# Kernel tuning notes

Measured on AMD Instinct MI355X. Metric: run time of the kernel, lower is better.

Reference implementation:

```python
import jax, jax.numpy as jnp
import numpy as np

N = 100000      # num nodes
E = 1000000     # num edges
R = 50          # num relations
B = 2           # num bases (hard-coded in source)
IN, HID, OUT = 128, 64, 64


def setup_inputs() -> dict:
    key = jax.random.key(0)
    ks = jax.random.split(key, 12)
    def xavier(k, shape):
        fan_in, fan_out = shape[-2], shape[-1]
        lim = (6.0 / (fan_in + fan_out)) ** 0.5
        return jax.random.uniform(k, shape, jnp.float32, -lim, lim)
    return {
        "node_emb": xavier(ks[0], (N, IN)),
        "basis1": xavier(ks[1], (B, IN, HID)),
        "comp1": xavier(ks[2], (R, B)),
        "loop_w1": xavier(ks[3], (IN, HID)),
        "bias1": jnp.zeros((HID,), jnp.float32),
        "basis2": xavier(ks[4], (B, HID, OUT)),
        "comp2": xavier(ks[5], (R, B)),
        "loop_w2": xavier(ks[6], (HID, OUT)),
        "bias2": jnp.zeros((OUT,), jnp.float32),
        "src": jax.random.randint(ks[7], (E,), 0, N, jnp.int32),
        "dst": jax.random.randint(ks[8], (E,), 0, N, jnp.int32),
        "etypes": jax.random.randint(ks[9], (E,), 0, R, jnp.int32),
    }


def _rel_graph_conv(h, basis, comp, loop_w, bias, src, dst, etypes, act):
    # Basis-decomposed R-GCN layer (DGL RelGraphConv, regularizer='basis'):
    #   W_r = sum_b comp[r,b] * basis[b];  m_e = W_{etype_e} h_{src_e}
    # Low-rank form: project with each basis first (2 dense GEMMs), then mix
    # per-edge with the relation coefficients, then scatter-add by dst.
    hb = jnp.einsum('nd,bdo->nbo', h, basis)          # [N, B, out]
    c = comp[etypes]                                   # [E, B]
    msg = jnp.einsum('eb,ebo->eo', c, hb[src])         # gather [E,B,out] -> [E,out]
    agg = jax.ops.segment_sum(msg, dst, num_segments=h.shape[0])  # scatter-add
    return act(agg + h @ loop_w + bias)                # self-loop + bias + activation


def reference(node_emb, basis1, comp1, loop_w1, bias1,
              basis2, comp2, loop_w2, bias2, src, dst, etypes):
    h = _rel_graph_conv(node_emb, basis1, comp1, loop_w1, bias1,
                        src, dst, etypes, jnp.tanh)
    out = _rel_graph_conv(h, basis2, comp2, loop_w2, bias2,
                          src, dst, etypes, jax.nn.relu)
    return out
```

## Files before the change

kernel.cpp:

```cpp
#include <hip/hip_runtime.h>
#include <math.h>


typedef short          short8 __attribute__((ext_vector_type(8)));
typedef float          f32x4  __attribute__((ext_vector_type(4)));
typedef unsigned short u16;

#define NCHUNK 256

static __device__ __forceinline__ u16 bf16_rne(float x) {
    unsigned u = __float_as_uint(x);
    return (u16)((u + 0x7fffu + ((u >> 16) & 1u)) >> 16);
}
static __device__ __forceinline__ float bf16_f32(u16 h) {
    return __uint_as_float(((unsigned)h) << 16);
}

__device__ __forceinline__ void wconv_body(
    int tid,
    const float* __restrict__ loopw1, const float* __restrict__ basis1,
    const float* __restrict__ loopw2, const float* __restrict__ basis2,
    u16* __restrict__ wt1h, u16* __restrict__ wt1l,
    u16* __restrict__ wt2h, u16* __restrict__ wt2l)
{
    if (tid < 192 * 128) {
        const int j = tid >> 7, k = tid & 127;
        const float w = (j < 64)
            ? loopw1[k * 64 + j]
            : basis1[(size_t)((j - 64) >> 6) * (128 * 64) + k * 64 + ((j - 64) & 63)];
        const u16 h = bf16_rne(w);
        wt1h[tid] = h;
        wt1l[tid] = bf16_rne(w - bf16_f32(h));
    }
    if (tid < 192 * 64) {
        const int j = tid >> 6, k = tid & 63;
        const float w = (j < 64)
            ? loopw2[k * 64 + j]
            : basis2[(size_t)((j - 64) >> 6) * (64 * 64) + k * 64 + ((j - 64) & 63)];
        const u16 h = bf16_rne(w);
        wt2h[tid] = h;
        wt2l[tid] = bf16_rne(w - bf16_f32(h));
    }
}

__global__ __launch_bounds__(256) void prep_count(
    const int* __restrict__ dst, int* __restrict__ cnt, int nE, int nB,
    const float* __restrict__ loopw1, const float* __restrict__ basis1,
    const float* __restrict__ loopw2, const float* __restrict__ basis2,
    u16* __restrict__ wt1h, u16* __restrict__ wt1l,
    u16* __restrict__ wt2h, u16* __restrict__ wt2l)
{
    const int t = threadIdx.x;
    if (blockIdx.x >= NCHUNK) {
        wconv_body((blockIdx.x - NCHUNK) * 256 + t,
                   loopw1, basis1, loopw2, basis2, wt1h, wt1l, wt2h, wt2l);
        return;
    }
    __shared__ int lh[1024];
    for (int b = t; b < 1024; b += 256) lh[b] = 0;
    __syncthreads();
    const int chunk = (nE + NCHUNK - 1) / NCHUNK;
    const int e0 = blockIdx.x * chunk;
    const int e1 = min(nE, e0 + chunk);
    for (int e = e0 + t; e < e1; e += 256)
        atomicAdd(&lh[dst[e] >> 7], 1);
    __syncthreads();
    for (int b = t; b < nB; b += 256)
        cnt[blockIdx.x * nB + b] = lh[b];
}

template<int K>
__global__ __launch_bounds__(512, 2) void rgcn_dense_mfma(
    const float* __restrict__ x,
    const u16* __restrict__ wth,
    const u16* __restrict__ wtl,
    const float* __restrict__ bias,
    float* __restrict__ self,
    unsigned* __restrict__ hbb,
    int nNodes)
{
    constexpr int KC  = K / 32;
    constexpr int GW  = K / 8;
    constexpr int GMW = GW - 1;
    __shared__ u16 wlds[96 * 2 * K];

    const int n0   = blockIdx.x * 128;
    const int lane = threadIdx.x & 63;
    const int w    = threadIdx.x >> 6;
    const int rl   = lane & 15;
    const int kb   = lane >> 4;

    const int row = n0 + w * 16 + rl;
    short8 Ah[KC], Al[KC];
    #pragma unroll
    for (int kc = 0; kc < KC; ++kc) {
        float v[8];
        if (row < nNodes) {
            const float* xp = x + (size_t)row * K + kc * 32 + kb * 8;
            const float4 a = *reinterpret_cast<const float4*>(xp);
            const float4 b = *reinterpret_cast<const float4*>(xp + 4);
            v[0] = a.x; v[1] = a.y; v[2] = a.z; v[3] = a.w;
            v[4] = b.x; v[5] = b.y; v[6] = b.z; v[7] = b.w;
        } else {
            #pragma unroll
            for (int i = 0; i < 8; ++i) v[i] = 0.f;
        }
        #pragma unroll
        for (int i = 0; i < 8; ++i) {
            const u16 h = bf16_rne(v[i]);
            Ah[kc][i] = (short)h;
            Al[kc][i] = (short)bf16_rne(v[i] - bf16_f32(h));
        }
    }

    f32x4 acc[12];
    #pragma unroll
    for (int j = 0; j < 12; ++j) acc[j] = (f32x4){0.f, 0.f, 0.f, 0.f};

    #pragma unroll
    for (int hf = 0; hf < 2; ++hf) {
        if (hf) __syncthreads();
        for (int gi = threadIdx.x; gi < 96 * 2 * GW; gi += 512) {
            const int ch = gi / (2 * GW);
            const int r  = gi - ch * 2 * GW;
            const int s  = r / GW;
            const int g  = r - s * GW;
            const u16* sp = (s == 0 ? wth : wtl)
                          + (size_t)(hf * 96 + ch) * K + g * 8;
            const short8 vv = *reinterpret_cast<const short8*>(sp);
            *reinterpret_cast<short8*>(
                &wlds[((ch * 2 + s) * GW + (g ^ (ch & GMW))) * 8]) = vv;
        }
        __syncthreads();

        #pragma unroll
        for (int j16h = 0; j16h < 6; ++j16h) {
            const int ch = j16h * 16 + rl;
            const u16* bbase = &wlds[(ch * 2) * GW * 8];
            #pragma unroll
            for (int kc = 0; kc < KC; ++kc) {
                const int gp = (kc * 4 + kb) ^ (ch & GMW);
                const short8 Bh =
                    *reinterpret_cast<const short8*>(bbase + gp * 8);
                const short8 Bl =
                    *reinterpret_cast<const short8*>(bbase + (GW + gp) * 8);
                f32x4 a = acc[hf * 6 + j16h];
                a = __builtin_amdgcn_mfma_f32_16x16x32_bf16(Ah[kc], Bh, a, 0, 0, 0);
                a = __builtin_amdgcn_mfma_f32_16x16x32_bf16(Ah[kc], Bl, a, 0, 0, 0);
                a = __builtin_amdgcn_mfma_f32_16x16x32_bf16(Al[kc], Bh, a, 0, 0, 0);
                acc[hf * 6 + j16h] = a;
            }
        }
    }

    const int rowbase = n0 + w * 16 + kb * 4;
    #pragma unroll
    for (int j16 = 0; j16 < 4; ++j16) {
        const float bj = bias[j16 * 16 + rl];
        #pragma unroll
        for (int r = 0; r < 4; ++r) {
            const int rr = rowbase + r;
            if (rr < nNodes)
                self[(size_t)rr * 64 + j16 * 16 + rl] = acc[j16][r] + bj;
        }
    }
    #pragma unroll
    for (int j16 = 4; j16 < 8; ++j16) {
        #pragma unroll
        for (int r = 0; r < 4; ++r) {
            const int rr = rowbase + r;
            if (rr < nNodes)
                hbb[(size_t)rr * 64 + (j16 - 4) * 16 + rl] =
                    (unsigned)bf16_rne(acc[j16][r])
                  | ((unsigned)bf16_rne(acc[j16 + 4][r]) << 16);
        }
    }
}

__global__ __launch_bounds__(NCHUNK) void bkt_chunkscan(
    int* __restrict__ cnt, int* __restrict__ tot, int nB)
{
    __shared__ int sm[NCHUNK];
    const int b = blockIdx.x, t = threadIdx.x;
    const int v = cnt[t * nB + b];
    sm[t] = v;
    __syncthreads();
    for (int off = 1; off < NCHUNK; off <<= 1) {
        const int u = (t >= off) ? sm[t - off] : 0;
        __syncthreads();
        sm[t] += u;
        __syncthreads();
    }
    cnt[t * nB + b] = sm[t] - v;
    if (t == NCHUNK - 1) tot[b] = sm[t];
}

__global__ __launch_bounds__(1024) void bkt_boff(
    const int* __restrict__ tot, int* __restrict__ boff, int nB, int nE)
{
    __shared__ int sm[1024];
    const int t = threadIdx.x;
    const int v = (t < nB) ? tot[t] : 0;
    sm[t] = v; __syncthreads();
    for (int off = 1; off < 1024; off <<= 1) {
        const int u = (t >= off) ? sm[t - off] : 0;
        __syncthreads();
        sm[t] += u;
        __syncthreads();
    }
    if (t < nB) boff[t] = sm[t] - v;
    if (t == 0) boff[nB] = nE;
}

__global__ __launch_bounds__(256) void bkt_scatter(
    const int* __restrict__ src, const int* __restrict__ dst,
    const int* __restrict__ et, const int* __restrict__ cnt,
    const int* __restrict__ boff, unsigned* __restrict__ rec,
    int nE, int nB)
{
    __shared__ int lcur[1024];
    const int t = threadIdx.x;
    const int c = blockIdx.x;
    for (int b = t; b < nB; b += 256)
        lcur[b] = boff[b] + cnt[c * nB + b];
    __syncthreads();
    const int chunk = (nE + NCHUNK - 1) / NCHUNK;
    const int e0 = c * chunk;
    const int e1 = min(nE, e0 + chunk);
    for (int e = e0 + t; e < e1; e += 256) {
        const int d = dst[e];
        const int p = atomicAdd(&lcur[d >> 7], 1);
        rec[p] = ((unsigned)(d & 127) << 23)
               | ((unsigned)src[e] << 6)
               | (unsigned)et[e];
    }
}

__global__ __launch_bounds__(256) void bkt_sort(
    const unsigned* __restrict__ rec, unsigned* __restrict__ rec2,
    const int* __restrict__ boff, int* __restrict__ rowptr,
    int nNodes)
{
    __shared__ int cnt[128];
    __shared__ int pos[128];
    const int b = blockIdx.x;
    const int t = threadIdx.x;
    const int beg = boff[b], end = boff[b + 1];
    if (t < 128) cnt[t] = 0;
    __syncthreads();
    for (int i = beg + t; i < end; i += 256)
        atomicAdd(&cnt[rec[i] >> 23], 1);
    __syncthreads();
    if (t < 128) pos[t] = cnt[t];
    __syncthreads();
    for (int off = 1; off < 128; off <<= 1) {
        int u = 0;
        if (t < 128 && t >= off) u = pos[t - off];
        __syncthreads();
        if (t < 128) pos[t] += u;
        __syncthreads();
    }
    if (t < 128) {
        const int ex = beg + pos[t] - cnt[t];
        pos[t] = ex;
        const int n = (b << 7) + t;
        if (n < nNodes) rowptr[n] = ex;
    }
    __syncthreads();
    for (int i = beg + t; i < end; i += 256) {
        const unsigned r = rec[i];
        const int p = atomicAdd(&pos[r >> 23], 1);
        rec2[p] = r;
    }
}

template<int ACT>
__global__ __launch_bounds__(256) void rgcn_agg(
    const unsigned* __restrict__ hbb,
    const float* __restrict__ comp,
    const int* __restrict__ rowptr,
    const unsigned* __restrict__ rec2,
    float* __restrict__ io,
    int nNodes, int nEdges)
{
    const int lane = threadIdx.x & 63;
    const int w  = (blockIdx.x * 256 + threadIdx.x) >> 6;
    const int nW = (gridDim.x * 256) >> 6;
    const float2* __restrict__ comp2 = reinterpret_cast<const float2*>(comp);
    for (int n = w; n < nNodes; n += nW) {
        const int beg = rowptr[n];
        const int end = (n == nNodes - 1) ? nEdges : rowptr[n + 1];
        const float self = io[(size_t)n * 64 + lane];
        float acc0 = 0.f, acc1 = 0.f;
        for (int base = beg; base < end; base += 64) {
            const int cnt = min(64, end - base);
            const unsigned r = (lane < cnt) ? rec2[base + lane] : 0u;
            int i = 0;
            for (; i + 8 <= cnt; i += 8) {
                int ss[8], tt[8];
                #pragma unroll
                for (int k = 0; k < 8; ++k) {
                    const unsigned rk = __shfl(r, i + k);
                    ss[k] = __builtin_amdgcn_readfirstlane(
                                (int)((rk >> 6) & 0x1FFFFu));
                    tt[k] = __builtin_amdgcn_readfirstlane((int)(rk & 63u));
                }
                unsigned v[8];
                #pragma unroll
                for (int k = 0; k < 8; ++k)
                    v[k] = hbb[(size_t)ss[k] * 64 + lane];
                #pragma unroll
                for (int k = 0; k < 8; ++k) {
                    const float2 c = comp2[tt[k]];
                    acc0 = fmaf(c.x, __uint_as_float(v[k] << 16), acc0);
                    acc1 = fmaf(c.y, __uint_as_float(v[k] & 0xffff0000u), acc1);
                }
            }
            for (; i + 2 <= cnt; i += 2) {
                const unsigned rA = __shfl(r, i), rB = __shfl(r, i + 1);
                const int sA = __builtin_amdgcn_readfirstlane(
                                   (int)((rA >> 6) & 0x1FFFFu));
                const int sB = __builtin_amdgcn_readfirstlane(
                                   (int)((rB >> 6) & 0x1FFFFu));
                const int tA = __builtin_amdgcn_readfirstlane((int)(rA & 63u));
                const int tB = __builtin_amdgcn_readfirstlane((int)(rB & 63u));
                const unsigned vA = hbb[(size_t)sA * 64 + lane];
                const unsigned vB = hbb[(size_t)sB * 64 + lane];
                const float2 cA = comp2[tA], cB = comp2[tB];
                acc0 = fmaf(cA.x, __uint_as_float(vA << 16), acc0);
                acc1 = fmaf(cA.y, __uint_as_float(vA & 0xffff0000u), acc1);
                acc0 = fmaf(cB.x, __uint_as_float(vB << 16), acc0);
                acc1 = fmaf(cB.y, __uint_as_float(vB & 0xffff0000u), acc1);
            }
            if (i < cnt) {
                const unsigned rA = __shfl(r, i);
                const int sA = __builtin_amdgcn_readfirstlane(
                                   (int)((rA >> 6) & 0x1FFFFu));
                const int tA = __builtin_amdgcn_readfirstlane((int)(rA & 63u));
                const unsigned vA = hbb[(size_t)sA * 64 + lane];
                const float2 cA = comp2[tA];
                acc0 = fmaf(cA.x, __uint_as_float(vA << 16), acc0);
                acc1 = fmaf(cA.y, __uint_as_float(vA & 0xffff0000u), acc1);
            }
        }
        float o = self + acc0 + acc1;
        o = (ACT == 0) ? tanhf(o) : fmaxf(o, 0.f);
        io[(size_t)n * 64 + lane] = o;
    }
}

extern "C" void kernel_launch(void* const* d_in, const int* in_sizes, int n_in,
                              void* d_out, int out_size, void* d_ws, size_t ws_size,
                              hipStream_t stream)
{
    const float* node_emb = (const float*)d_in[0];
    const float* basis1   = (const float*)d_in[1];
    const float* comp1    = (const float*)d_in[2];
    const float* loop_w1  = (const float*)d_in[3];
    const float* bias1    = (const float*)d_in[4];
    const float* basis2   = (const float*)d_in[5];
    const float* comp2    = (const float*)d_in[6];
    const float* loop_w2  = (const float*)d_in[7];
    const float* bias2    = (const float*)d_in[8];
    const int*   src      = (const int*)d_in[9];
    const int*   dst      = (const int*)d_in[10];
    const int*   et       = (const int*)d_in[11];

    const int N = in_sizes[0] / 128;
    const int E = in_sizes[9];
    const int nB = (N + 127) / 128;

    float* out = (float*)d_out;

    unsigned* hbb    = (unsigned*)d_ws;
    float*    h      = (float*)(hbb + (size_t)N * 64);
    unsigned* rec    = (unsigned*)(h + (size_t)N * 64);
    unsigned* rec2   = rec + E;
    int*      cnt    = (int*)(rec2 + E);
    int*      tot    = cnt + NCHUNK * nB;
    int*      boff   = tot + nB;
    int*      rowptr = boff + nB + 1;
    u16*      wt1h   = (u16*)(rowptr + N);
    u16*      wt1l   = wt1h + 192 * 128;
    u16*      wt2h   = wt1l + 192 * 128;
    u16*      wt2l   = wt2h + 192 * 64;

    const int nBlkDense = (N + 127) / 128;
    const int nBlkAgg   = (N + 3) / 4;

    prep_count<<<NCHUNK + 96, 256, 0, stream>>>(
        dst, cnt, E, nB, loop_w1, basis1, loop_w2, basis2,
        wt1h, wt1l, wt2h, wt2l);

    bkt_chunkscan<<<nB, NCHUNK, 0, stream>>>(cnt, tot, nB);
    bkt_boff     <<<1,    1024, 0, stream>>>(tot, boff, nB, E);
    bkt_scatter  <<<NCHUNK, 256, 0, stream>>>(src, dst, et, cnt, boff, rec, E, nB);
    bkt_sort     <<<nB,     256, 0, stream>>>(rec, rec2, boff, rowptr, N);

    rgcn_dense_mfma<128><<<nBlkDense, 512, 0, stream>>>(
        node_emb, wt1h, wt1l, bias1, h, hbb, N);
    rgcn_agg<0><<<nBlkAgg, 256, 0, stream>>>(
        hbb, comp1, rowptr, rec2, h, N, E);

    rgcn_dense_mfma<64><<<nBlkDense, 512, 0, stream>>>(
        h, wt2h, wt2l, bias2, out, hbb, N);
    rgcn_agg<1><<<nBlkAgg, 256, 0, stream>>>(
        hbb, comp2, rowptr, rec2, out, N, E);
}
```

Measured before the change: 189.8 us.

## Shrink dense MFMA blocks and batch 16 gathers per step in aggregation

The dense MFMA kernel now uses 256-thread blocks covering 64 rows and stages the weight columns through LDS in four 48-column chunks instead of two 96-column halves. This halves the LDS footprint and allows more blocks per CU, at the cost of reloading the weights more often overall. The aggregation kernel replaces its 8/2/1 tail loops with a single loop that issues 16 gathers per step, using readlane for the source and type indices and predicating the FMAs. This exposes more memory-level parallelism per wave but can issue redundant loads past the end of short rows.

```diff
diff --git a/kernel.cpp b/kernel.cpp
--- a/kernel.cpp
+++ b/kernel.cpp
@@ -70,7 +70,7 @@
 }
 
 template<int K>
-__global__ __launch_bounds__(512, 2) void rgcn_dense_mfma(
+__global__ __launch_bounds__(256, 4) void rgcn_dense_mfma(
     const float* __restrict__ x,
     const u16* __restrict__ wth,
     const u16* __restrict__ wtl,
@@ -82,9 +82,9 @@
     constexpr int KC  = K / 32;
     constexpr int GW  = K / 8;
     constexpr int GMW = GW - 1;
-    __shared__ u16 wlds[96 * 2 * K];
-
-    const int n0   = blockIdx.x * 128;
+    __shared__ u16 wlds[48 * 2 * K];
+
+    const int n0   = blockIdx.x * 64;
     const int lane = threadIdx.x & 63;
     const int w    = threadIdx.x >> 6;
     const int rl   = lane & 15;
@@ -118,15 +118,15 @@
     for (int j = 0; j < 12; ++j) acc[j] = (f32x4){0.f, 0.f, 0.f, 0.f};
 
     #pragma unroll
-    for (int hf = 0; hf < 2; ++hf) {
-        if (hf) __syncthreads();
-        for (int gi = threadIdx.x; gi < 96 * 2 * GW; gi += 512) {
+    for (int cc = 0; cc < 4; ++cc) {
+        if (cc) __syncthreads();
+        for (int gi = threadIdx.x; gi < 48 * 2 * GW; gi += 256) {
             const int ch = gi / (2 * GW);
-            const int r  = gi - ch * 2 * GW;
-            const int s  = r / GW;
-            const int g  = r - s * GW;
+            const int r2 = gi - ch * 2 * GW;
+            const int s  = r2 / GW;
+            const int g  = r2 - s * GW;
             const u16* sp = (s == 0 ? wth : wtl)
-                          + (size_t)(hf * 96 + ch) * K + g * 8;
+                          + (size_t)(cc * 48 + ch) * K + g * 8;
             const short8 vv = *reinterpret_cast<const short8*>(sp);
             *reinterpret_cast<short8*>(
                 &wlds[((ch * 2 + s) * GW + (g ^ (ch & GMW))) * 8]) = vv;
@@ -134,7 +134,7 @@
         __syncthreads();
 
         #pragma unroll
-        for (int j16h = 0; j16h < 6; ++j16h) {
+        for (int j16h = 0; j16h < 3; ++j16h) {
             const int ch = j16h * 16 + rl;
             const u16* bbase = &wlds[(ch * 2) * GW * 8];
             #pragma unroll
@@ -144,11 +144,11 @@
                     *reinterpret_cast<const short8*>(bbase + gp * 8);
                 const short8 Bl =
                     *reinterpret_cast<const short8*>(bbase + (GW + gp) * 8);
-                f32x4 a = acc[hf * 6 + j16h];
+                f32x4 a = acc[cc * 3 + j16h];
                 a = __builtin_amdgcn_mfma_f32_16x16x32_bf16(Ah[kc], Bh, a, 0, 0, 0);
                 a = __builtin_amdgcn_mfma_f32_16x16x32_bf16(Ah[kc], Bl, a, 0, 0, 0);
                 a = __builtin_amdgcn_mfma_f32_16x16x32_bf16(Al[kc], Bh, a, 0, 0, 0);
-                acc[hf * 6 + j16h] = a;
+                acc[cc * 3 + j16h] = a;
             }
         }
     }
@@ -295,52 +295,23 @@
         for (int base = beg; base < end; base += 64) {
             const int cnt = min(64, end - base);
             const unsigned r = (lane < cnt) ? rec2[base + lane] : 0u;
-            int i = 0;
-            for (; i + 8 <= cnt; i += 8) {
-                int ss[8], tt[8];
+            for (int i = 0; i < cnt; i += 16) {
+                unsigned v[16]; int tt[16];
                 #pragma unroll
-                for (int k = 0; k < 8; ++k) {
-                    const unsigned rk = __shfl(r, i + k);
-                    ss[k] = __builtin_amdgcn_readfirstlane(
-                                (int)((rk >> 6) & 0x1FFFFu));
-                    tt[k] = __builtin_amdgcn_readfirstlane((int)(rk & 63u));
+                for (int k = 0; k < 16; ++k) {
+                    const unsigned rk =
+                        (unsigned)__builtin_amdgcn_readlane((int)r, i + k);
+                    tt[k] = (int)(rk & 63u);
+                    v[k] = hbb[(size_t)((rk >> 6) & 0x1FFFFu) * 64 + lane];
                 }
-                unsigned v[8];
                 #pragma unroll
-                for (int k = 0; k < 8; ++k)
-                    v[k] = hbb[(size_t)ss[k] * 64 + lane];
-                #pragma unroll
-                for (int k = 0; k < 8; ++k) {
-                    const float2 c = comp2[tt[k]];
-                    acc0 = fmaf(c.x, __uint_as_float(v[k] << 16), acc0);
-                    acc1 = fmaf(c.y, __uint_as_float(v[k] & 0xffff0000u), acc1);
+                for (int k = 0; k < 16; ++k) {
+                    if (i + k < cnt) {
+                        const float2 c = comp2[tt[k]];
+                        acc0 = fmaf(c.x, __uint_as_float(v[k] << 16), acc0);
+                        acc1 = fmaf(c.y, __uint_as_float(v[k] & 0xffff0000u), acc1);
+                    }
                 }
-            }
-            for (; i + 2 <= cnt; i += 2) {
-                const unsigned rA = __shfl(r, i), rB = __shfl(r, i + 1);
-                const int sA = __builtin_amdgcn_readfirstlane(
-                                   (int)((rA >> 6) & 0x1FFFFu));
-                const int sB = __builtin_amdgcn_readfirstlane(
-                                   (int)((rB >> 6) & 0x1FFFFu));
-                const int tA = __builtin_amdgcn_readfirstlane((int)(rA & 63u));
-                const int tB = __builtin_amdgcn_readfirstlane((int)(rB & 63u));
-                const unsigned vA = hbb[(size_t)sA * 64 + lane];
-                const unsigned vB = hbb[(size_t)sB * 64 + lane];
-                const float2 cA = comp2[tA], cB = comp2[tB];
-                acc0 = fmaf(cA.x, __uint_as_float(vA << 16), acc0);
-                acc1 = fmaf(cA.y, __uint_as_float(vA & 0xffff0000u), acc1);
-                acc0 = fmaf(cB.x, __uint_as_float(vB << 16), acc0);
-                acc1 = fmaf(cB.y, __uint_as_float(vB & 0xffff0000u), acc1);
-            }
-            if (i < cnt) {
-                const unsigned rA = __shfl(r, i);
-                const int sA = __builtin_amdgcn_readfirstlane(
-                                   (int)((rA >> 6) & 0x1FFFFu));
-                const int tA = __builtin_amdgcn_readfirstlane((int)(rA & 63u));
-                const unsigned vA = hbb[(size_t)sA * 64 + lane];
-                const float2 cA = comp2[tA];
-                acc0 = fmaf(cA.x, __uint_as_float(vA << 16), acc0);
-                acc1 = fmaf(cA.y, __uint_as_float(vA & 0xffff0000u), acc1);
             }
         }
         float o = self + acc0 + acc1;
@@ -385,7 +356,7 @@
     u16*      wt2h   = wt1l + 192 * 128;
     u16*      wt2l   = wt2h + 192 * 64;
 
-    const int nBlkDense = (N + 127) / 128;
+    const int nBlkDense = (N + 63) / 64;
     const int nBlkAgg   = (N + 3) / 4;
 
     prep_count<<<NCHUNK + 96, 256, 0, stream>>>(
@@ -397,12 +368,12 @@
     bkt_scatter  <<<NCHUNK, 256, 0, stream>>>(src, dst, et, cnt, boff, rec, E, nB);
     bkt_sort     <<<nB,     256, 0, stream>>>(rec, rec2, boff, rowptr, N);
 
-    rgcn_dense_mfma<128><<<nBlkDense, 512, 0, stream>>>(
+    rgcn_dense_mfma<128><<<nBlkDense, 256, 0, stream>>>(
         node_emb, wt1h, wt1l, bias1, h, hbb, N);
     rgcn_agg<0><<<nBlkAgg, 256, 0, stream>>>(
         hbb, comp1, rowptr, rec2, h, N, E);
 
-    rgcn_dense_mfma<64><<<nBlkDense, 512, 0, stream>>>(
+    rgcn_dense_mfma<64><<<nBlkDense, 256, 0, stream>>>(
         h, wt2h, wt2l, bias2, out, hbb, N);
     rgcn_agg<1><<<nBlkAgg, 256, 0, stream>>>(
         hbb, comp2, rowptr, rec2, out, N, E);
```

New measurement: 200.5 us. +5.6%, slower.
